# Optimization experiments

Hardware: AMD Instinct MI355X
Metric: run time of the kernel (lower is better)

Reference implementation:

```python
import jax, jax.numpy as jnp
import numpy as np
from jax import lax

NUM_CLASSES = 5
K_MAX = 5
PROTO_DIM = 32
MARGIN = 1.0
ANCHOR_STRENGTH = 1.0
LAMBDA_COMPACT = 0.1
MAX_ANCHORS = 2048
KMEANS_ITERS = 5
EPS = 1e-12


def _normalize(x, axis=-1):
    return x / jnp.sqrt(jnp.sum(x * x, axis=axis, keepdims=True) + EPS)


def _cdist(a, b):
    # Euclidean distance matrix (n, m) via the squared-norm expansion.
    d2 = (jnp.sum(a * a, 1)[:, None] + jnp.sum(b * b, 1)[None, :] - 2.0 * (a @ b.T))
    return jnp.sqrt(jnp.maximum(d2, 0.0))


def _class_centroids(feats, mask, key):
    # feats: (N, D) L2-normalized; mask: (N,) bool selecting this class's voxels.
    N, D = feats.shape
    w = mask.astype(feats.dtype)
    cnt = w.sum()
    mean = (feats * w[:, None]).sum(0) / jnp.maximum(cnt, 1.0)

    def kmeans(_):
        k_init, k_fb = jax.random.split(key)
        # random init: K distinct masked points (gumbel top-k == randperm sample)
        g0 = jax.random.gumbel(k_init, (N,))
        _, init_idx = lax.top_k(jnp.where(mask, g0, -jnp.inf), K_MAX)
        cent0 = feats[init_idx]
        # fallback random masked points for empty clusters, one set per iter
        g2 = jax.random.gumbel(k_fb, (KMEANS_ITERS, N))
        fb_idx = jax.vmap(lambda s: lax.top_k(jnp.where(mask, s, -jnp.inf), K_MAX)[1])(g2)

        def body(cent, fb):
            d = _cdist(feats, cent)                       # (N, K)
            assign = jnp.argmin(d, axis=1)
            onehot = ((assign[:, None] == jnp.arange(K_MAX)[None, :]) & mask[:, None]).astype(feats.dtype)
            counts = onehot.sum(0)                        # (K,)
            sums = onehot.T @ feats                       # (K, D)
            newc = sums / jnp.maximum(counts, 1.0)[:, None]
            newc = jnp.where(counts[:, None] > 0, newc, feats[fb])
            return newc, None

        cent, _ = lax.scan(body, cent0, fb_idx)
        return _normalize(cent)

    def mean_rep(_):
        return jnp.tile(mean[None, :], (K_MAX, 1))

    cent = lax.cond(cnt >= K_MAX, kmeans, mean_rep, None)
    return _normalize(cent), cnt


def _loss_triplet(feats, prototypes, pseudo_masks, gt_masks, labeled_batch):
    B, Df, Zf, Yf, Xf = feats.shape
    N = B * Zf * Yf * Xf
    feats_flat = _normalize(jnp.transpose(feats, (0, 2, 3, 4, 1)).reshape(N, Df))
    # masks are already at feature resolution -> nearest interp is identity
    gt_flat = gt_masks.reshape(-1)
    pseudo_flat = pseudo_masks.reshape(-1)
    protos = _normalize(prototypes)                       # (C, K, D)
    key = jax.random.key(42)

    # ---- anchor loss: match prototypes to per-class kmeans centroids ----
    anchor_loss = jnp.float32(0.0)
    anchor_cnt = jnp.float32(0.0)
    for i in range(int(labeled_batch.shape[0])):
        c = labeled_batch[i]
        c_safe = jnp.clip(c, 0, NUM_CLASSES - 1)
        cmask = gt_flat == c
        cent, cnt = _class_centroids(feats_flat, cmask, jax.random.fold_in(key, i))
        valid = ((c != 0) & (c < NUM_CLASSES) & (cnt > 0)).astype(jnp.float32)
        loss_c = jnp.mean((protos[c_safe] - cent) ** 2)
        anchor_loss = anchor_loss + valid * loss_c
        anchor_cnt = anchor_cnt + valid
    anchor_loss = anchor_loss / jnp.maximum(anchor_cnt, 1.0)

    # ---- compactness: unbiased variance across the K prototypes per class ----
    compact_loss = jnp.var(protos[1:], axis=1, ddof=1).mean(axis=1).sum()

    # ---- triplet loss over pseudo-labeled anchors ----
    amask = pseudo_flat > 0
    ga = jax.random.gumbel(jax.random.fold_in(key, 1000), (N,))
    top_s, aidx = lax.top_k(jnp.where(amask, ga, -jnp.inf), MAX_ANCHORS)
    sel_valid = jnp.isfinite(top_s)                        # padding if < MAX_ANCHORS anchors
    a_feats = feats_flat[aidx]                             # (A, D)
    a_labels = jnp.clip(pseudo_flat[aidx], 0, NUM_CLASSES - 1)

    CK = NUM_CLASSES * K_MAX
    protos_flat = protos.reshape(CK, Df)
    col_cls = jnp.arange(CK) // K_MAX
    own = col_cls[None, :] == a_labels[:, None]            # (A, CK)

    sim = a_feats @ protos_flat.T
    pos_idx = jnp.argmax(jnp.where(own, sim, -jnp.inf), axis=1)
    pos_vecs = protos_flat[pos_idx]

    d_all = _cdist(a_feats, protos_flat)                   # (A, CK)
    pos_d = jnp.min(jnp.where(own, d_all, jnp.inf), axis=1)
    neg = ~own
    semi = neg & (d_all > pos_d[:, None]) & (d_all < pos_d[:, None] + MARGIN)
    g1 = jax.random.gumbel(jax.random.fold_in(key, 2000), (MAX_ANCHORS, CK))
    g2 = jax.random.gumbel(jax.random.fold_in(key, 2001), (MAX_ANCHORS, CK))
    idx_semi = jnp.argmax(jnp.where(semi, g1, -jnp.inf), axis=1)
    idx_rand = jnp.argmax(jnp.where(neg, g2, -jnp.inf), axis=1)
    neg_idx = jnp.where(semi.any(axis=1), idx_semi, idx_rand)
    neg_vecs = protos_flat[neg_idx]

    aN, pN, nN = _normalize(a_feats), _normalize(pos_vecs), _normalize(neg_vecs)
    d_pos = jnp.sqrt(jnp.sum((aN - pN) ** 2, axis=1) + EPS)
    d_neg = jnp.sqrt(jnp.sum((aN - nN) ** 2, axis=1) + EPS)
    wA = (sel_valid & (a_labels != 0)).astype(jnp.float32)
    proto_loss = jnp.sum(jax.nn.softplus(d_pos - d_neg + MARGIN) * wA) / jnp.maximum(wA.sum(), 1.0)

    return proto_loss + ANCHOR_STRENGTH * anchor_loss + LAMBDA_COMPACT * compact_loss


def setup_inputs() -> dict:
    key = jax.random.key(0)
    k1, k2, k3, k4 = jax.random.split(key, 4)
    B, Z = 4, 64
    feats = jax.random.normal(k1, (B, PROTO_DIM, Z, Z, Z), dtype=jnp.float32)
    protos = jax.random.normal(k2, (NUM_CLASSES, K_MAX, PROTO_DIM), dtype=jnp.float32)
    protos = _normalize(protos)
    pseudo_masks = jax.random.randint(k3, (B, Z, Z, Z), 0, NUM_CLASSES, dtype=jnp.int32)
    gt_masks = jax.random.randint(k4, (B, Z, Z, Z), 0, NUM_CLASSES, dtype=jnp.int32)
    labeled_batch = jnp.array([1, 2, 3, 4], dtype=jnp.int32)
    return {"feats": feats, "prototypes": protos, "pseudo_masks": pseudo_masks,
            "gt_masks": gt_masks, "labeled_batch": labeled_batch}


def reference(feats, prototypes, pseudo_masks, gt_masks, labeled_batch):
    return _loss_triplet(feats, prototypes, pseudo_masks, gt_masks, labeled_batch)
```

## Files before the change

kernel.cpp:

```cpp
#include <hip/hip_runtime.h>
#include <hip/hip_fp16.h>
#include <stdint.h>

typedef unsigned int u32;
typedef unsigned long long u64;
typedef unsigned char u8;

#define NCLS 5
#define KMX 5
#define DD 32
#define LBN 4
#define KIT 5
#define MAXA 2048
#define CKK 25
#define NBLKA 256
#define SCPAD 36
#define ACAP 4096
#define UKTHR ((1u << 23) + 1u - (1u << 15))
#define FTINY 1.17549435e-38f

struct RKeys {
  u32 ki[LBN][2];
  u32 kf[LBN][2];
  u32 k1000[2];
  u32 k2000[2];
  u32 k2001[2];
};

struct SelState {
  u32 prefix1, rank1, prefix21, rank2, pivot_sv, target, M, ncand, ncand2;
};

__host__ __device__ inline void tf2x32(u32 k0, u32 k1, u32 x0, u32 x1, u32* o0, u32* o1) {
  u32 ks2 = k0 ^ k1 ^ 0x1BD11BDAu;
  u32 ks[3] = {k0, k1, ks2};
  x0 += k0; x1 += k1;
  const int rotA[4] = {13, 15, 26, 6};
  const int rotB[4] = {17, 29, 16, 24};
#pragma unroll
  for (int g = 0; g < 5; ++g) {
#pragma unroll
    for (int j = 0; j < 4; ++j) {
      int r = (g & 1) ? rotB[j] : rotA[j];
      x0 += x1;
      x1 = (x1 << r) | (x1 >> (32 - r));
      x1 ^= x0;
    }
    x0 += ks[(g + 1) % 3];
    x1 += ks[(g + 2) % 3] + (u32)(g + 1);
  }
  *o0 = x0; *o1 = x1;
}

__device__ inline u32 jax_ukey(u32 k0, u32 k1, u32 half, u32 idx) {
  bool hi = (idx >= half);
  u32 c0 = hi ? (idx - half) : idx;
  u32 c1 = hi ? idx : (idx + half);
  u32 o0, o1;
  tf2x32(k0, k1, c0, c1, &o0, &o1);
  u32 bits = hi ? o1 : o0;
  return (bits >> 9) + 1u;
}

#define INS5(kk, a0, a1, a2, a3, a4) do { u64 _k = (kk); \
  if (_k > a4) { a4 = _k; u64 _t; \
    if (a4 > a3) { _t = a3; a3 = a4; a4 = _t; } \
    if (a3 > a2) { _t = a2; a2 = a3; a3 = _t; } \
    if (a2 > a1) { _t = a1; a1 = a2; a2 = _t; } \
    if (a1 > a0) { _t = a0; a0 = a1; a1 = _t; } } } while (0)

#define WMERGE5(off, a0, a1, a2, a3, a4) do { \
  u64 r0 = __shfl_xor(a0, off, 64), r1 = __shfl_xor(a1, off, 64), \
      r2 = __shfl_xor(a2, off, 64), r3 = __shfl_xor(a3, off, 64), \
      r4 = __shfl_xor(a4, off, 64); \
  INS5(r0, a0, a1, a2, a3, a4); INS5(r1, a0, a1, a2, a3, a4); \
  INS5(r2, a0, a1, a2, a3, a4); INS5(r3, a0, a1, a2, a3, a4); \
  INS5(r4, a0, a1, a2, a3, a4); } while (0)

#define WMERGE_ALL(a0,a1,a2,a3,a4) do { \
  WMERGE5(32,a0,a1,a2,a3,a4); WMERGE5(16,a0,a1,a2,a3,a4); WMERGE5(8,a0,a1,a2,a3,a4); \
  WMERGE5(4,a0,a1,a2,a3,a4); WMERGE5(2,a0,a1,a2,a3,a4); WMERGE5(1,a0,a1,a2,a3,a4); } while (0)

__device__ inline float rsum32(float v) {
#pragma unroll
  for (int o = 16; o; o >>= 1) v += __shfl_xor(v, o, 32);
  return v;
}

__device__ inline float rsum64(float v) {
#pragma unroll
  for (int o = 32; o; o >>= 1) v += __shfl_xor(v, o, 64);
  return v;
}

__device__ inline float4 h8tof4(uint2 u) {
  __half2 a = *reinterpret_cast<__half2*>(&u.x);
  __half2 b = *reinterpret_cast<__half2*>(&u.y);
  float2 fa = __half22float2(a), fb = __half22float2(b);
  return make_float4(fa.x, fa.y, fb.x, fb.y);
}
__device__ inline uint2 f4toh8(float4 f) {
  __half2 a = __float22half2_rn(make_float2(f.x, f.y));
  __half2 b = __float22half2_rn(make_float2(f.z, f.w));
  uint2 u;
  u.x = *reinterpret_cast<u32*>(&a);
  u.y = *reinterpret_cast<u32*>(&b);
  return u;
}


__global__ void k_protos(const float* __restrict__ protos, float* __restrict__ protn, float* __restrict__ compact) {
  __shared__ float pl[CKK * DD];
  __shared__ float rn[CKK];
  __shared__ float red[4];
  int tid = threadIdx.x;
  for (int t = tid; t < CKK * DD; t += 256) pl[t] = protos[t];
  __syncthreads();
  if (tid < CKK) {
    float s = 0.f;
    for (int d = 0; d < DD; ++d) { float x = pl[tid * DD + d]; s += x * x; }
    rn[tid] = sqrtf(s + 1e-12f);
  }
  __syncthreads();
  for (int t = tid; t < CKK * DD; t += 256) {
    float v = pl[t] / rn[t / DD];
    pl[t] = v;
    protn[t] = v;
  }
  __syncthreads();
  float part = 0.f;
  if (tid < (NCLS - 1) * DD) {
    int c = 1 + tid / DD;
    int d = tid % DD;
    float m = 0.f;
#pragma unroll
    for (int k = 0; k < KMX; ++k) m += pl[(c * KMX + k) * DD + d];
    m *= (1.0f / KMX);
    float v = 0.f;
#pragma unroll
    for (int k = 0; k < KMX; ++k) { float df = pl[(c * KMX + k) * DD + d] - m; v += df * df; }
    part = v * (1.0f / (KMX - 1)) * (1.0f / DD);
  }
#pragma unroll
  for (int o = 32; o; o >>= 1) part += __shfl_xor(part, o, 64);
  int wid = tid >> 6;
  if ((tid & 63) == 0) red[wid] = part;
  __syncthreads();
  if (tid == 0) compact[0] = red[0] + red[1] + red[2] + red[3];
}


#define T5PROC_THR(gv_, nn_, cv_) do { \
  int ci = (gv_ == lb0) ? 0 : (gv_ == lb1) ? 1 : (gv_ == lb2) ? 2 : (gv_ == lb3) ? 3 : -1; \
  cv_ = (u8)(ci < 0 ? 255 : ci); \
  if (ci >= 0) { \
    u32 k0 = (ci & 2) ? ((ci & 1) ? ka3 : ka2) : ((ci & 1) ? ka1 : ka0); \
    u32 k1 = (ci & 2) ? ((ci & 1) ? kb3 : kb2) : ((ci & 1) ? kb1 : kb0); \
    u32 uk = jax_ukey(k0, k1, half, (u32)(nn_)); \
    if (uk >= UKTHR) { \
      u64 key = ((u64)uk << 32) | (u32)(~(u32)(nn_)); \
      if (ci == 0) { INS5(key, A0, A1, A2, A3, A4); } \
      else if (ci == 1) { INS5(key, B0, B1, B2, B3, B4); } \
      else if (ci == 2) { INS5(key, C0, C1, C2, C3, C4); } \
      else { INS5(key, D0, D1, D2, D3, D4); } \
    } \
  } } while (0)

#define T5PROC(gv_, nn_) do { \
  int ci = (gv_ == lb0) ? 0 : (gv_ == lb1) ? 1 : (gv_ == lb2) ? 2 : (gv_ == lb3) ? 3 : -1; \
  if (ci >= 0) { \
    u32 k0 = (ci & 2) ? ((ci & 1) ? ka3 : ka2) : ((ci & 1) ? ka1 : ka0); \
    u32 k1 = (ci & 2) ? ((ci & 1) ? kb3 : kb2) : ((ci & 1) ? kb1 : kb0); \
    u32 uk = jax_ukey(k0, k1, half, (u32)(nn_)); \
    u64 key = ((u64)uk << 32) | (u32)(~(u32)(nn_)); \
    if (ci == 0) { INS5(key, A0, A1, A2, A3, A4); } \
    else if (ci == 1) { INS5(key, B0, B1, B2, B3, B4); } \
    else if (ci == 2) { INS5(key, C0, C1, C2, C3, C4); } \
    else { INS5(key, D0, D1, D2, D3, D4); } \
  } } while (0)

#define T5_TAIL_STORE() \
  WMERGE_ALL(A0,A1,A2,A3,A4); \
  WMERGE_ALL(B0,B1,B2,B3,B4); \
  WMERGE_ALL(C0,C1,C2,C3,C4); \
  WMERGE_ALL(D0,D1,D2,D3,D4); \
  __shared__ u64 wbuf[4][20]; \
  int tid = threadIdx.x; \
  int wid = tid >> 6; \
  if ((tid & 63) == 0) { \
    u64* w = wbuf[wid]; \
    w[0]=A0; w[1]=A1; w[2]=A2; w[3]=A3; w[4]=A4; \
    w[5]=B0; w[6]=B1; w[7]=B2; w[8]=B3; w[9]=B4; \
    w[10]=C0; w[11]=C1; w[12]=C2; w[13]=C3; w[14]=C4; \
    w[15]=D0; w[16]=D1; w[17]=D2; w[18]=D3; w[19]=D4; \
  } \
  __syncthreads(); \
  if (tid == 0) { \
    _Pragma("unroll") \
    for (int w = 1; w < 4; ++w) { \
      _Pragma("unroll") \
      for (int j = 0; j < 5; ++j) { \
        u64 ka = wbuf[w][j];      INS5(ka, A0, A1, A2, A3, A4); \
        u64 kb = wbuf[w][5 + j];  INS5(kb, B0, B1, B2, B3, B4); \
        u64 kc = wbuf[w][10 + j]; INS5(kc, C0, C1, C2, C3, C4); \
        u64 kd = wbuf[w][15 + j]; INS5(kd, D0, D1, D2, D3, D4); \
      } \
    } \
    size_t nb = gridDim.x; \
    u64* o0 = outA + ((size_t)0 * nb + blockIdx.x) * 5; \
    o0[0]=A0; o0[1]=A1; o0[2]=A2; o0[3]=A3; o0[4]=A4; \
    u64* o1 = outA + ((size_t)1 * nb + blockIdx.x) * 5; \
    o1[0]=B0; o1[1]=B1; o1[2]=B2; o1[3]=B3; o1[4]=B4; \
    u64* o2 = outA + ((size_t)2 * nb + blockIdx.x) * 5; \
    o2[0]=C0; o2[1]=C1; o2[2]=C2; o2[3]=C3; o2[4]=C4; \
    u64* o3 = outA + ((size_t)3 * nb + blockIdx.x) * 5; \
    o3[0]=D0; o3[1]=D1; o3[2]=D2; o3[3]=D3; o3[4]=D4; \
  }

#define T5_HEAD() \
  int lb0 = labeled[0], lb1 = labeled[1], lb2 = labeled[2], lb3 = labeled[3]; \
  u32 half = (u32)(N / 2); \
  u32 ka0 = RK.ki[0][0], kb0 = RK.ki[0][1]; \
  u32 ka1 = RK.ki[1][0], kb1 = RK.ki[1][1]; \
  u32 ka2 = RK.ki[2][0], kb2 = RK.ki[2][1]; \
  u32 ka3 = RK.ki[3][0], kb3 = RK.ki[3][1]; \
  u64 A0=0,A1=0,A2=0,A3=0,A4=0; \
  u64 B0=0,B1=0,B2=0,B3=0,B4=0; \
  u64 C0=0,C1=0,C2=0,C3=0,C4=0; \
  u64 D0=0,D1=0,D2=0,D3=0,D4=0;

__global__ void k_top5A(const int* __restrict__ gt, const int* __restrict__ labeled,
                        RKeys RK, u64* __restrict__ outA, u8* __restrict__ ci8, int N) {
  T5_HEAD()
  int Nq = N >> 2;
  int stride = gridDim.x * blockDim.x;
  for (int q = blockIdx.x * blockDim.x + threadIdx.x; q < Nq; q += stride) {
    int4 g4 = ((const int4*)gt)[q];
    int n = q << 2;
    u8 c0v, c1v, c2v, c3v;
    T5PROC_THR(g4.x, n, c0v);
    T5PROC_THR(g4.y, n + 1, c1v);
    T5PROC_THR(g4.z, n + 2, c2v);
    T5PROC_THR(g4.w, n + 3, c3v);
    ((uchar4*)ci8)[q] = make_uchar4(c0v, c1v, c2v, c3v);
  }
  T5_TAIL_STORE()
}

__global__ void k_top5B(const u64* __restrict__ outA, u32* __restrict__ rescue,
                        u64* __restrict__ top5F, int nblk) {
  int i = blockIdx.x;
  const u64* src = outA + (size_t)i * nblk * 5;
  u64 t0 = 0, t1 = 0, t2 = 0, t3 = 0, t4 = 0;
  int tot = nblk * 5;
  for (int j = threadIdx.x; j < tot; j += blockDim.x) { u64 k = src[j]; INS5(k, t0, t1, t2, t3, t4); }
  WMERGE_ALL(t0, t1, t2, t3, t4);
  __shared__ u64 wbuf[4 * 5];
  int tid = threadIdx.x;
  int wid = tid >> 6;
  if ((tid & 63) == 0) {
    wbuf[wid * 5 + 0] = t0; wbuf[wid * 5 + 1] = t1; wbuf[wid * 5 + 2] = t2;
    wbuf[wid * 5 + 3] = t3; wbuf[wid * 5 + 4] = t4;
  }
  __syncthreads();
  if (tid == 0) {
#pragma unroll
    for (int w = 1; w < 4; ++w)
#pragma unroll
      for (int j = 0; j < 5; ++j) { u64 k = wbuf[w * 5 + j]; INS5(k, t0, t1, t2, t3, t4); }
    u64* o = top5F + (size_t)i * 5;
    o[0] = t0; o[1] = t1; o[2] = t2; o[3] = t3; o[4] = t4;
    if (t4 == 0ULL) atomicOr(rescue, 1u << i);
  }
}

__global__ void k_top5A_resc(const int* __restrict__ gt, const int* __restrict__ labeled,
                             RKeys RK, const u32* __restrict__ rescue,
                             u64* __restrict__ outA, int N) {
  if ((rescue[0] & 0xFu) == 0u) return;
  T5_HEAD()
  int Nq = N >> 2;
  int stride = gridDim.x * blockDim.x;
  for (int q = blockIdx.x * blockDim.x + threadIdx.x; q < Nq; q += stride) {
    int4 g4 = ((const int4*)gt)[q];
    int n = q << 2;
    T5PROC(g4.x, n);
    T5PROC(g4.y, n + 1);
    T5PROC(g4.z, n + 2);
    T5PROC(g4.w, n + 3);
  }
  T5_TAIL_STORE()
}

__global__ void k_top5B_resc(const u64* __restrict__ outA, const u32* __restrict__ rescue,
                             u64* __restrict__ top5F, int nblk) {
  int i = blockIdx.x;
  if (!((rescue[0] >> i) & 1u)) return;
  const u64* src = outA + (size_t)i * nblk * 5;
  u64 t0 = 0, t1 = 0, t2 = 0, t3 = 0, t4 = 0;
  int tot = nblk * 5;
  for (int j = threadIdx.x; j < tot; j += blockDim.x) { u64 k = src[j]; INS5(k, t0, t1, t2, t3, t4); }
  WMERGE_ALL(t0, t1, t2, t3, t4);
  __shared__ u64 wbuf[4 * 5];
  int tid = threadIdx.x;
  int wid = tid >> 6;
  if ((tid & 63) == 0) {
    wbuf[wid * 5 + 0] = t0; wbuf[wid * 5 + 1] = t1; wbuf[wid * 5 + 2] = t2;
    wbuf[wid * 5 + 3] = t3; wbuf[wid * 5 + 4] = t4;
  }
  __syncthreads();
  if (tid == 0) {
#pragma unroll
    for (int w = 1; w < 4; ++w)
#pragma unroll
      for (int j = 0; j < 5; ++j) { u64 k = wbuf[w * 5 + j]; INS5(k, t0, t1, t2, t3, t4); }
    u64* o = top5F + (size_t)i * 5;
    o[0] = t0; o[1] = t1; o[2] = t2; o[3] = t3; o[4] = t4;
  }
}


__global__ void __launch_bounds__(256)
k_normT(const float4* __restrict__ feats4, uint2* __restrict__ featsH2, int N, int Z3) {
  __shared__ float xl[128 * 33];
  __shared__ float sinv[128];
  int tid = threadIdx.x;
  int nchunk = N >> 7;
  int Z3q = Z3 >> 2;
  for (int chunk = blockIdx.x; chunk < nchunk; chunk += gridDim.x) {
    int n0 = chunk << 7;
    int b = n0 / Z3, v0 = n0 - b * Z3;
    const float4* fb4 = feats4 + (size_t)b * DD * Z3q + (v0 >> 2);
#pragma unroll
    for (int j = 0; j < 4; ++j) {
      int idx = j * 256 + tid;
      int d = idx >> 5, v4 = idx & 31;
      float4 f = fb4[(size_t)d * Z3q + v4];
      int vb = v4 << 2;
      xl[(vb + 0) * 33 + d] = f.x;
      xl[(vb + 1) * 33 + d] = f.y;
      xl[(vb + 2) * 33 + d] = f.z;
      xl[(vb + 3) * 33 + d] = f.w;
    }
    __syncthreads();
    if (tid < 128) {
      float s = 0.f;
#pragma unroll
      for (int d = 0; d < DD; ++d) { float x = xl[tid * 33 + d]; s += x * x; }
      sinv[tid] = 1.0f / sqrtf(s + 1e-12f);
    }
    __syncthreads();
#pragma unroll
    for (int j = 0; j < 4; ++j) {
      int idx = j * 256 + tid;
      int vox = idx >> 3, q = idx & 7;
      float iv = sinv[vox];
      float4 o;
      o.x = xl[vox * 33 + q * 4 + 0] * iv;
      o.y = xl[vox * 33 + q * 4 + 1] * iv;
      o.z = xl[vox * 33 + q * 4 + 2] * iv;
      o.w = xl[vox * 33 + q * 4 + 3] * iv;
      featsH2[(size_t)n0 * 8 + idx] = f4toh8(o);
    }
    __syncthreads();
  }
}

__global__ void k_initcentT(const u32* __restrict__ featsH,
                            const u64* __restrict__ top5F, float* __restrict__ cent, int N) {
  int t = threadIdx.x;
  if (t >= LBN * KMX * DD) return;
  int d = t & 31;
  int k = (t >> 5) % KMX;
  int i = t / (KMX * DD);
  u32 n = ~(u32)(top5F[(size_t)i * 5 + k]);
  if (n >= (u32)N) n = 0;
  const __half* fh = (const __half*)featsH;
  cent[(i * KMX + k) * DD + d] = __half2float(fh[(size_t)n * DD + d]);
}

__global__ void __launch_bounds__(256)
k_assignW2(const uint2* __restrict__ featsH2, const u8* __restrict__ ci8,
           const float* __restrict__ cent, float* __restrict__ part, int N, int NB) {
  __shared__ float sc[LBN * KMX * SCPAD];
  __shared__ float ssw[8][LBN * KMX * SCPAD];
  __shared__ float scn[LBN * KMX];
  __shared__ float scw[8][LBN * KMX];
  int tid = threadIdx.x;
  for (int t = tid; t < LBN * KMX * DD; t += 256) {
    int cl2 = t >> 5, d = t & 31;
    sc[cl2 * SCPAD + d] = cent[t];
  }
  for (int t = tid; t < 8 * LBN * KMX * SCPAD; t += 256) (&ssw[0][0])[t] = 0.f;
  for (int t = tid; t < 8 * LBN * KMX; t += 256) (&scw[0][0])[t] = 0.f;
  __syncthreads();
  if (tid < LBN * KMX) {
    float s = 0.f;
#pragma unroll
    for (int d = 0; d < DD; ++d) { float c = sc[tid * SCPAD + d]; s += c * c; }
    scn[tid] = s;
  }
  __syncthreads();
  int q = tid & 7;
  int grp = (tid >> 3) & 7;
  int wv = tid >> 6;
  int cpi = 2 * wv + (grp >> 2);
  float* myss = &ssw[cpi][0];
  float* mysc = &scw[cpi][0];
  int sstep = grp & 3;
  const float* scq = sc + q * 4;
  int nchunk = N >> 5;
  int chunk = blockIdx.x;
  if (chunk < nchunk) {
    uint2 h2 = featsH2[(size_t)chunk * 256 + tid];
    int cv = ci8[(chunk << 5) + (tid >> 3)];
    while (true) {
      int nxt = chunk + gridDim.x;
      bool has = nxt < nchunk;
      uint2 nh2 = make_uint2(0u, 0u); int ncv = 255;
      if (has) {
        nh2 = featsH2[(size_t)nxt * 256 + tid];
        ncv = ci8[(nxt << 5) + (tid >> 3)];
      }
      float4 f4 = h8tof4(h2);
      int ci = (cv == 255) ? -1 : cv;
      int basec = (ci < 0 ? 0 : ci) * KMX;
      float4 c0 = *(const float4*)(scq + (basec + 0) * SCPAD);
      float4 c1 = *(const float4*)(scq + (basec + 1) * SCPAD);
      float4 c2 = *(const float4*)(scq + (basec + 2) * SCPAD);
      float4 c3 = *(const float4*)(scq + (basec + 3) * SCPAD);
      float4 c4 = *(const float4*)(scq + (basec + 4) * SCPAD);
      float p0 = f4.x * c0.x + f4.y * c0.y + f4.z * c0.z + f4.w * c0.w;
      float p1 = f4.x * c1.x + f4.y * c1.y + f4.z * c1.z + f4.w * c1.w;
      float p2 = f4.x * c2.x + f4.y * c2.y + f4.z * c2.z + f4.w * c2.w;
      float p3 = f4.x * c3.x + f4.y * c3.y + f4.z * c3.z + f4.w * c3.w;
      float p4 = f4.x * c4.x + f4.y * c4.y + f4.z * c4.z + f4.w * c4.w;
#pragma unroll
      for (int o = 1; o < 8; o <<= 1) {
        p0 += __shfl_xor(p0, o, 64);
        p1 += __shfl_xor(p1, o, 64);
        p2 += __shfl_xor(p2, o, 64);
        p3 += __shfl_xor(p3, o, 64);
        p4 += __shfl_xor(p4, o, 64);
      }
      float bd = scn[basec + 0] - 2.0f * p0; int bk = 0;
      float d2;
      d2 = scn[basec + 1] - 2.0f * p1; if (d2 < bd) { bd = d2; bk = 1; }
      d2 = scn[basec + 2] - 2.0f * p2; if (d2 < bd) { bd = d2; bk = 2; }
      d2 = scn[basec + 3] - 2.0f * p3; if (d2 < bd) { bd = d2; bk = 3; }
      d2 = scn[basec + 4] - 2.0f * p4; if (d2 < bd) { bd = d2; bk = 4; }
      int cl = basec + bk;
#pragma unroll
      for (int s = 0; s < 4; ++s) {
        if (sstep == s && ci >= 0) {
          float* dst = myss + cl * SCPAD + q * 4;
          float4 cur = *(float4*)dst;
          cur.x += f4.x; cur.y += f4.y; cur.z += f4.z; cur.w += f4.w;
          *(float4*)dst = cur;
          if (q == 0) mysc[cl] += 1.0f;
        }
      }
      if (!has) break;
      chunk = nxt; h2 = nh2; cv = ncv;
    }
  }
  __syncthreads();
  for (int p = tid; p < 660; p += 256) {
    float v;
    if (p < 640) {
      int idx = (p >> 5) * SCPAD + (p & 31);
      v = ssw[0][idx] + ssw[1][idx] + ssw[2][idx] + ssw[3][idx]
        + ssw[4][idx] + ssw[5][idx] + ssw[6][idx] + ssw[7][idx];
    } else {
      int ik = p - 640;
      v = scw[0][ik] + scw[1][ik] + scw[2][ik] + scw[3][ik]
        + scw[4][ik] + scw[5][ik] + scw[6][ik] + scw[7][ik];
    }
    part[(size_t)p * NB + blockIdx.x] = v;
  }
}

__global__ void k_redupdT(const float* __restrict__ part, float* __restrict__ cent,
                          float* __restrict__ sums, float* __restrict__ kcnt,
                          u32* __restrict__ emptyMask, int NB) {
  __shared__ float w4[8];
  int p = blockIdx.x;
  int tid = threadIdx.x;
  if (p < 640) {
    int ik = p >> 5;
    float s = 0.f, c = 0.f;
    for (int b2 = tid; b2 < NB; b2 += 256) {
      s += part[(size_t)p * NB + b2];
      c += part[(size_t)(640 + ik) * NB + b2];
    }
    s = rsum64(s); c = rsum64(c);
    int wid = tid >> 6;
    if ((tid & 63) == 0) { w4[wid] = s; w4[4 + wid] = c; }
    __syncthreads();
    if (tid == 0) {
      float S = w4[0] + w4[1] + w4[2] + w4[3];
      float C = w4[4] + w4[5] + w4[6] + w4[7];
      sums[p] = S;
      if (C > 0.f) cent[p] = S / fmaxf(C, 1.0f);
      else atomicOr(emptyMask, 1u << ik);
    }
  } else if (p < 660) {
    int ik = p - 640;
    float c = 0.f;
    for (int b2 = tid; b2 < NB; b2 += 256) c += part[(size_t)(640 + ik) * NB + b2];
    c = rsum64(c);
    int wid = tid >> 6;
    if ((tid & 63) == 0) w4[wid] = c;
    __syncthreads();
    if (tid == 0) kcnt[ik] = w4[0] + w4[1] + w4[2] + w4[3];
  }
}

__global__ void __launch_bounds__(1024)
k_fixempty(const u32* __restrict__ featsH, const int* __restrict__ gt,
           const int* __restrict__ labeled, RKeys RK, u32* __restrict__ emptyMask,
           float* __restrict__ cent, int iter, int N) {
  u32 mask = emptyMask[0];
  if (mask == 0u) return;
  __shared__ u64 wbuf[16 * 5];
  __shared__ u32 idxs[KMX];
  int tid = threadIdx.x;
  u32 halfF = (u32)(((u64)5 * (u64)N) / 2);
  for (int ci = 0; ci < LBN; ++ci) {
    if (((mask >> (ci * KMX)) & 0x1Fu) == 0u) continue;
    int c = labeled[ci];
    u32 fa = RK.kf[ci][0], fb = RK.kf[ci][1];
    u32 base = (u32)iter * (u32)N;
    u64 t0 = 0, t1 = 0, t2 = 0, t3 = 0, t4 = 0;
    for (int n = tid; n < N; n += 1024) {
      if (gt[n] != c) continue;
      u32 uk = jax_ukey(fa, fb, halfF, base + (u32)n);
      u64 key = ((u64)uk << 32) | (u32)(~(u32)n);
      INS5(key, t0, t1, t2, t3, t4);
    }
    WMERGE_ALL(t0, t1, t2, t3, t4);
    int wid = tid >> 6;
    if ((tid & 63) == 0) {
      wbuf[wid * 5 + 0] = t0; wbuf[wid * 5 + 1] = t1; wbuf[wid * 5 + 2] = t2;
      wbuf[wid * 5 + 3] = t3; wbuf[wid * 5 + 4] = t4;
    }
    __syncthreads();
    if (tid == 0) {
      for (int w = 1; w < 16; ++w)
        for (int j = 0; j < 5; ++j) { u64 k = wbuf[w * 5 + j]; INS5(k, t0, t1, t2, t3, t4); }
      idxs[0] = ~(u32)t0; idxs[1] = ~(u32)t1; idxs[2] = ~(u32)t2;
      idxs[3] = ~(u32)t3; idxs[4] = ~(u32)t4;
    }
    __syncthreads();
    if (tid < KMX * DD) {
      int k = tid >> 5, d = tid & 31;
      if ((mask >> (ci * KMX + k)) & 1u) {
        u32 n = idxs[k];
        if (n >= (u32)N) n = 0;
        const __half* fh = (const __half*)featsH;
        cent[(ci * KMX + k) * DD + d] = __half2float(fh[(size_t)n * DD + d]);
      }
    }
    __syncthreads();
  }
  if (tid == 0) emptyMask[0] = 0u;
}

__global__ void k_prepT(const uint2* __restrict__ featsH2,
                        const int* __restrict__ pseudo, const SelState* __restrict__ st,
                        const int* __restrict__ aidx, float4* __restrict__ afe4,
                        int* __restrict__ alab, int N) {
  int tid = threadIdx.x;
  int r = blockIdx.x * 32 + (tid >> 3);
  int q = tid & 7;
  if (r >= (int)st->target) return;
  int n = aidx[r];
  if ((u32)n >= (u32)N) n = 0;
  if (q == 0) {
    int lb = pseudo[n];
    alab[r] = lb < 0 ? 0 : (lb > NCLS - 1 ? NCLS - 1 : lb);
  }
  afe4[(size_t)r * 8 + q] = h8tof4(featsH2[(size_t)n * 8 + q]);
}


__global__ void __launch_bounds__(256)
k_anchsel(const int* __restrict__ pseudo, RKeys RK, u64* __restrict__ cand4k,
          SelState* st, int N) {
  __shared__ u32 mcnt[4];
  u32 K0 = RK.k1000[0], K1 = RK.k1000[1];
  u32 half = (u32)(N / 2);
  int tid = threadIdx.x;
  int lcnt = 0;
  int stride = gridDim.x * blockDim.x;
  for (int n = blockIdx.x * blockDim.x + tid; n < N; n += stride) {
    bool valid = pseudo[n] > 0;
    lcnt += valid ? 1 : 0;
    u32 uk = jax_ukey(K0, K1, half, (u32)n);
    bool c = valid && (uk >= UKTHR);
    if (__ballot(c)) {
      if (c) {
        u32 p = atomicAdd(&st->ncand, 1u);
        if (p < (u32)ACAP) cand4k[p] = ((u64)uk << 32) | (u32)(~(u32)n);
      }
    }
  }
#pragma unroll
  for (int o = 32; o; o >>= 1) lcnt += __shfl_xor(lcnt, o, 64);
  if ((tid & 63) == 0) mcnt[tid >> 6] = (u32)lcnt;
  __syncthreads();
  if (tid == 0) atomicAdd(&st->M, mcnt[0] + mcnt[1] + mcnt[2] + mcnt[3]);
}

__global__ void k_selmode(SelState* st, u32* rescue) {
  if (threadIdx.x != 0 || blockIdx.x != 0) return;
  u32 M = st->M;
  u32 tgt = M < (u32)MAXA ? M : (u32)MAXA;
  st->target = tgt;
  if (!(st->ncand >= tgt && st->ncand <= (u32)ACAP)) rescue[1] = 1u;
}

__global__ void __launch_bounds__(256)
k_rank(const u64* __restrict__ cand4k, const SelState* __restrict__ st,
       const u32* __restrict__ rescue, int* __restrict__ aidx) {
  if (rescue[1]) return;
  __shared__ u64 keys[ACAP];
  u32 nc = st->ncand; if (nc > (u32)ACAP) nc = (u32)ACAP;
  u32 target = st->target;
  int tid = threadIdx.x;
  for (int t = tid; t < ACAP; t += 256) keys[t] = (t < (int)nc) ? cand4k[t] : 0ULL;
  __syncthreads();
  int i = blockIdx.x * 256 + tid;
  if (i >= (int)nc) return;
  u64 my = keys[i];
  u32 rank = 0;
  for (u32 j = 0; j < nc; ++j) rank += (keys[j] > my) ? 1u : 0u;
  if (rank < target) aidx[rank] = (int)(~(u32)my);
}


__global__ void k_svinit(const int* __restrict__ pseudo, RKeys RK, const u32* __restrict__ rescue,
                         u32* __restrict__ sv, u32* __restrict__ hist, int N) {
  if (!rescue[1]) return;
  __shared__ u32 h[2048];
  for (int t = threadIdx.x; t < 2048; t += blockDim.x) h[t] = 0;
  __syncthreads();
  u32 half = (u32)(N / 2);
  u32 K0 = RK.k1000[0], K1 = RK.k1000[1];
  int Nq = N >> 2;
  int stride = gridDim.x * blockDim.x;
  for (int q = blockIdx.x * blockDim.x + threadIdx.x; q < Nq; q += stride) {
    int4 p4 = ((const int4*)pseudo)[q];
    int n = q << 2;
    u32 s0 = 0, s1 = 0, s2 = 0, s3 = 0;
    if (p4.x > 0) { s0 = jax_ukey(K0, K1, half, (u32)n);     atomicAdd(&h[s0 >> 21], 1u); }
    if (p4.y > 0) { s1 = jax_ukey(K0, K1, half, (u32)n + 1); atomicAdd(&h[s1 >> 21], 1u); }
    if (p4.z > 0) { s2 = jax_ukey(K0, K1, half, (u32)n + 2); atomicAdd(&h[s2 >> 21], 1u); }
    if (p4.w > 0) { s3 = jax_ukey(K0, K1, half, (u32)n + 3); atomicAdd(&h[s3 >> 21], 1u); }
    ((uint4*)sv)[q] = make_uint4(s0, s1, s2, s3);
  }
  __syncthreads();
  for (int t = threadIdx.x; t < 2048; t += blockDim.x) if (h[t]) atomicAdd(&hist[t], h[t]);
}

__global__ void k_hist12(const u32* __restrict__ sv, u32* __restrict__ hist,
                         const SelState* __restrict__ st, const u32* __restrict__ rescue,
                         int pass, int N) {
  if (!rescue[1]) return;
  __shared__ u32 h[2048];
  for (int t = threadIdx.x; t < 2048; t += blockDim.x) h[t] = 0;
  __syncthreads();
  u32 pre = (pass == 1) ? st->prefix1 : st->prefix21;
  int Nq = N >> 2;
  int stride = gridDim.x * blockDim.x;
  for (int q = blockIdx.x * blockDim.x + threadIdx.x; q < Nq; q += stride) {
    uint4 s4 = ((const uint4*)sv)[q];
#define H12(s_) do { u32 s = (s_); if (s) { \
      if (pass == 1) { if ((s >> 21) == pre) atomicAdd(&h[(s >> 10) & 0x7FFu], 1u); } \
      else           { if ((s >> 10) == pre) atomicAdd(&h[s & 0x3FFu], 1u); } } } while (0)
    H12(s4.x); H12(s4.y); H12(s4.z); H12(s4.w);
#undef H12
  }
  __syncthreads();
  for (int t = threadIdx.x; t < 2048; t += blockDim.x) if (h[t]) atomicAdd(&hist[t], h[t]);
}

__global__ void k_scan(const u32* __restrict__ hist, SelState* st,
                       const u32* __restrict__ rescue, int pass) {
  if (!rescue[1]) return;
  __shared__ u32 h[2048];
  __shared__ u32 csum[256];
  __shared__ u32 sh_rank;
  __shared__ int sh_found;
  __shared__ u32 sh_rem;
  int tid = threadIdx.x;
  int nb = (pass == 2) ? 1024 : 2048;
  for (int t = tid; t < 2048; t += 256) h[t] = (t < nb) ? hist[t] : 0u;
  __syncthreads();
  u32 cs = 0;
#pragma unroll
  for (int j = 0; j < 8; ++j) cs += h[tid * 8 + j];
  csum[tid] = cs;
  __syncthreads();
  if (tid == 0) {
    sh_rank = (pass == 0) ? st->target : (pass == 1 ? st->rank1 : st->rank2);
    sh_found = -1;
    sh_rem = 0;
  }
  __syncthreads();
  u32 rank = sh_rank;
  if (rank > 0) {
    u32 above = 0;
    for (int j = tid + 1; j < 256; ++j) above += csum[j];
    u32 run = above;
    for (int b = tid * 8 + 7; b >= tid * 8; --b) {
      u32 c = h[b];
      if (run < rank && rank <= run + c) { sh_found = b; sh_rem = rank - run; }
      run += c;
    }
  }
  __syncthreads();
  if (tid == 0) {
    int found = sh_found;
    u32 rem = sh_rem;
    if (pass == 0) {
      if (found < 0) { st->prefix1 = 0xFFFFFFFFu; st->rank1 = 0; }
      else { st->prefix1 = (u32)found; st->rank1 = rem; }
    } else if (pass == 1) {
      if (found < 0) { st->prefix21 = 0xFFFFFFFFu; st->rank2 = 0; }
      else { st->prefix21 = (st->prefix1 << 11) | (u32)found; st->rank2 = rem; }
    } else {
      if (found < 0) st->pivot_sv = 0xFFFFFFFFu;
      else st->pivot_sv = (st->prefix21 << 10) | (u32)found;
    }
  }
}

__global__ void k_gather(const u32* __restrict__ sv, SelState* st,
                         const u32* __restrict__ rescue, u64* __restrict__ cand, int N) {
  if (!rescue[1]) return;
  if (st->target == 0) return;
  u32 piv = st->pivot_sv;
  int Nq = N >> 2;
  int stride = gridDim.x * blockDim.x;
  for (int q = blockIdx.x * blockDim.x + threadIdx.x; q < Nq; q += stride) {
    uint4 s4 = ((const uint4*)sv)[q];
    int n = q << 2;
#define GPUSH(s_, nn_) do { u32 s = (s_); \
    if (s && s >= piv) { u32 p = atomicAdd(&st->ncand2, 1u); \
      if (p < 4096u) cand[p] = ((u64)s << 32) | (u32)(~(u32)(nn_)); } } while (0)
    GPUSH(s4.x, n); GPUSH(s4.y, n + 1); GPUSH(s4.z, n + 2); GPUSH(s4.w, n + 3);
#undef GPUSH
  }
}

__global__ void __launch_bounds__(1024) k_sortsel(const u64* __restrict__ cand,
                                                  const SelState* __restrict__ st,
                                                  const u32* __restrict__ rescue,
                                                  int* __restrict__ aidx) {
  if (!rescue[1]) return;
  __shared__ u64 s[4096];
  u32 nc = st->ncand2; if (nc > 4096u) nc = 4096u;
  u32 target = st->target;
  for (int t = threadIdx.x; t < 4096; t += blockDim.x) s[t] = (t < (int)nc) ? cand[t] : 0ULL;
  __syncthreads();
  for (u32 ksz = 2; ksz <= 4096; ksz <<= 1) {
    for (u32 j = ksz >> 1; j > 0; j >>= 1) {
      for (u32 idx = threadIdx.x; idx < 4096; idx += blockDim.x) {
        u32 ixj = idx ^ j;
        if (ixj > idx) {
          bool up = (idx & ksz) == 0;
          u64 A = s[idx], B = s[ixj];
          bool sw = up ? (A < B) : (A > B);
          if (sw) { s[idx] = B; s[ixj] = A; }
        }
      }
      __syncthreads();
    }
  }
  for (int t = threadIdx.x; t < MAXA; t += blockDim.x)
    if (t < (int)target) aidx[t] = (int)(~(u32)s[t]);
}


__global__ void k_anchor_final(const float* __restrict__ cent, const float* __restrict__ sums,
                               const float* __restrict__ kcnt, const float* __restrict__ protn,
                               const int* __restrict__ labeled, float* __restrict__ accum) {
  int i = blockIdx.x;
  int d = threadIdx.x;
  if (d >= DD) return;
  int c = labeled[i];
  float cnt = 0.f;
#pragma unroll
  for (int k = 0; k < KMX; ++k) cnt += kcnt[i * KMX + k];
  int cs = c < 0 ? 0 : (c > NCLS - 1 ? NCLS - 1 : c);
  float part = 0.f;
  if (cnt >= (float)KMX) {
#pragma unroll
    for (int k = 0; k < KMX; ++k) {
      float v = cent[(i * KMX + k) * DD + d];
      float s = rsum32(v * v);
      float dn1 = sqrtf(s + 1e-12f);
      float v1 = v / dn1;
      float s2 = rsum32(v1 * v1);
      float dn2 = sqrtf(s2 + 1e-12f);
      float vv = v1 / dn2;
      float df = protn[(cs * KMX + k) * DD + d] - vv;
      part += df * df;
    }
  } else {
    float mv = 0.f;
#pragma unroll
    for (int k = 0; k < KMX; ++k) mv += sums[(i * KMX + k) * DD + d];
    mv /= fmaxf(cnt, 1.0f);
    float s = rsum32(mv * mv);
    float dn = sqrtf(s + 1e-12f);
    float vv = mv / dn;
#pragma unroll
    for (int k = 0; k < KMX; ++k) {
      float df = protn[(cs * KMX + k) * DD + d] - vv;
      part += df * df;
    }
  }
  float ls = rsum32(part) * (1.0f / (KMX * DD));
  bool valid = (c != 0) && (c < NCLS) && (cnt > 0.f);
  if (d == 0 && valid) { atomicAdd(&accum[0], ls); atomicAdd(&accum[1], 1.0f); }
}

__global__ void k_triplet(const float* __restrict__ protn, const float* __restrict__ afe,
                          const int* __restrict__ alab, const SelState* __restrict__ st,
                          RKeys RK, float* __restrict__ acc) {
  __shared__ float pn[CKK * DD];
  __shared__ float spn[CKK];
  int tid = threadIdx.x;
  for (int t = tid; t < CKK * DD; t += blockDim.x) pn[t] = protn[t];
  __syncthreads();
  if (tid < CKK) {
    float s = 0.f;
    for (int d = 0; d < DD; ++d) s += pn[tid * DD + d] * pn[tid * DD + d];
    spn[tid] = s;
  }
  __syncthreads();
  int r = blockIdx.x * blockDim.x + tid;
  if (r >= (int)st->target) return;
  float a[DD]; float sa = 0.f;
#pragma unroll
  for (int d = 0; d < DD; ++d) { a[d] = afe[(size_t)r * DD + d]; sa += a[d] * a[d]; }
  int lab = alab[r];
  int ob = lab * KMX;
  float bs = -3.4e38f; int pidx = ob;
  float pos_d = 3.4e38f;
  for (int k = ob; k < ob + KMX; ++k) {
    float dot = 0.f;
#pragma unroll
    for (int d = 0; d < DD; ++d) dot += a[d] * pn[k * DD + d];
    if (dot > bs) { bs = dot; pidx = k; }
    float d2 = (sa + spn[k]) - 2.0f * dot;
    float dd = sqrtf(fmaxf(d2, 0.f));
    pos_d = fminf(pos_d, dd);
  }
  u32 halfT = (u32)(MAXA * CKK / 2);
  bool any_semi = false;
  u32 bu1 = 0; int k1i = 0;
  u32 bu2 = 0; int k2i = 0;
  for (int k = 0; k < CKK; ++k) {
    if (k / KMX == lab) continue;
    float dot = 0.f;
#pragma unroll
    for (int d = 0; d < DD; ++d) dot += a[d] * pn[k * DD + d];
    float d2 = (sa + spn[k]) - 2.0f * dot;
    float dd = sqrtf(fmaxf(d2, 0.f));
    u32 j = (u32)(r * CKK + k);
    bool semi = (dd > pos_d) && (dd < pos_d + 1.0f);
    if (semi) {
      u32 u1 = jax_ukey(RK.k2000[0], RK.k2000[1], halfT, j);
      any_semi = true;
      if (u1 > bu1) { bu1 = u1; k1i = k; }
    }
    u32 u2 = jax_ukey(RK.k2001[0], RK.k2001[1], halfT, j);
    if (u2 > bu2) { bu2 = u2; k2i = k; }
  }
  int nidx = any_semi ? k1i : k2i;
  float aden = sqrtf(sa + 1e-12f);
  float pden = sqrtf(spn[pidx] + 1e-12f);
  float nden = sqrtf(spn[nidx] + 1e-12f);
  float s1 = 0.f, s2 = 0.f;
#pragma unroll
  for (int d = 0; d < DD; ++d) {
    float an = a[d] / aden;
    float pv = pn[pidx * DD + d] / pden;
    float nv = pn[nidx * DD + d] / nden;
    float t1 = an - pv; s1 += t1 * t1;
    float t2 = an - nv; s2 += t2 * t2;
  }
  float d_pos = sqrtf(s1 + 1e-12f);
  float d_neg = sqrtf(s2 + 1e-12f);
  float xx = (d_pos - d_neg) + 1.0f;
  float l = fmaxf(xx, 0.f) + log1pf(expf(-fabsf(xx)));
  atomicAdd(&acc[0], l);
  atomicAdd(&acc[1], 1.0f);
}

__global__ void k_final(const float* __restrict__ anchor_acc, const float* __restrict__ proto_acc,
                        const float* __restrict__ compact, float* __restrict__ out) {
  if (threadIdx.x != 0 || blockIdx.x != 0) return;
  float al = anchor_acc[0] / fmaxf(anchor_acc[1], 1.0f);
  float pl = proto_acc[0] / fmaxf(proto_acc[1], 1.0f);
  out[0] = pl + 1.0f * al + 0.1f * compact[0];
}


static void host_keys(RKeys* K) {
  const u32 b0 = 0u, b1 = 42u;
  u32 o0, o1;
  for (int i = 0; i < LBN; ++i) {
    u32 f0, f1;
    tf2x32(b0, b1, 0u, (u32)i, &f0, &f1);
    u32 p0, q0, p1, q1;
    tf2x32(f0, f1, 0u, 2u, &p0, &q0);
    tf2x32(f0, f1, 1u, 3u, &p1, &q1);
    K->ki[i][0] = p0; K->ki[i][1] = p1;
    K->kf[i][0] = q0; K->kf[i][1] = q1;
  }
  tf2x32(b0, b1, 0u, 1000u, &o0, &o1); K->k1000[0] = o0; K->k1000[1] = o1;
  tf2x32(b0, b1, 0u, 2000u, &o0, &o1); K->k2000[0] = o0; K->k2000[1] = o1;
  tf2x32(b0, b1, 0u, 2001u, &o0, &o1); K->k2001[0] = o0; K->k2001[1] = o1;
}

extern "C" void kernel_launch(void* const* d_in, const int* in_sizes, int n_in,
                              void* d_out, int out_size, void* d_ws, size_t ws_size,
                              hipStream_t stream) {
  const float* feats = (const float*)d_in[0];
  const float* protos = (const float*)d_in[1];
  const int* pseudo = (const int*)d_in[2];
  const int* gt = (const int*)d_in[3];
  const int* labeled = (const int*)d_in[4];
  float* out = (float*)d_out;

  int N = in_sizes[2];
  int Z3 = N / 4;

  RKeys RK;
  host_keys(&RK);

  const int nbas[3] = {1536, 768, 384};
  for (int attempt = 0; attempt < 3; ++attempt) {
    int NBAS = nbas[attempt];
    char* W = (char*)d_ws;
    size_t off = 0;
    auto alloc = [&](size_t bytes) -> char* {
      char* p = W + off;
      off += (bytes + 255) & ~(size_t)255;
      return p;
    };
    char* zeroBase = W + off;
    u32* hist3 = (u32*)alloc(3 * 2048 * 4);
    SelState* st = (SelState*)alloc(256);
    float* anchor_acc = (float*)alloc(256);
    float* proto_acc = (float*)alloc(256);
    u32* rescue = (u32*)alloc(256);
    size_t zeroBytes = (size_t)((W + off) - zeroBase);
    u64* cand4k = (u64*)alloc((size_t)ACAP * 8);
    u64* outA = (u64*)alloc((size_t)LBN * NBLKA * 5 * 8);
    u64* top5F = (u64*)alloc((size_t)LBN * 5 * 8);
    float* cent = (float*)alloc((size_t)LBN * KMX * DD * 4);
    float* sums = (float*)alloc((size_t)LBN * KMX * DD * 4);
    float* kcnt = (float*)alloc((size_t)LBN * KMX * 4);
    float* protn = (float*)alloc((size_t)CKK * DD * 4);
    float* compact = (float*)alloc(256);
    u32* sv = (u32*)alloc((size_t)N * 4);
    float* part = (float*)alloc((size_t)680 * NBAS * 4);
    u64* cand = (u64*)alloc(4096 * 8);
    int* aidx = (int*)alloc((size_t)MAXA * 4);
    int* alab = (int*)alloc((size_t)MAXA * 4);
    float* afe = (float*)alloc((size_t)MAXA * DD * 4);
    u32* featsH = (u32*)alloc((size_t)N * DD * 2);
    u8* ci8 = (u8*)alloc((size_t)N);
    if (ws_size < off) continue;

    hipMemsetAsync(zeroBase, 0, zeroBytes, stream);

    k_protos<<<dim3(1), dim3(256), 0, stream>>>(protos, protn, compact);

    k_top5A<<<dim3(NBLKA), dim3(256), 0, stream>>>(gt, labeled, RK, outA, ci8, N);
    k_top5B<<<dim3(LBN), dim3(256), 0, stream>>>(outA, rescue, top5F, NBLKA);
    k_top5A_resc<<<dim3(NBLKA), dim3(256), 0, stream>>>(gt, labeled, RK, rescue, outA, N);
    k_top5B_resc<<<dim3(LBN), dim3(256), 0, stream>>>(outA, rescue, top5F, NBLKA);

    uint2* featsH2 = (uint2*)featsH;
    k_normT<<<dim3(4096), dim3(256), 0, stream>>>((const float4*)feats, featsH2, N, Z3);
    k_initcentT<<<dim3(1), dim3(LBN * KMX * DD), 0, stream>>>(featsH, top5F, cent, N);
    for (int it = 0; it < KIT; ++it) {
      k_assignW2<<<dim3(NBAS), dim3(256), 0, stream>>>(featsH2, ci8, cent, part, N, NBAS);
      k_redupdT<<<dim3(660), dim3(256), 0, stream>>>(part, cent, sums, kcnt, rescue + 2, NBAS);
      k_fixempty<<<dim3(1), dim3(1024), 0, stream>>>(featsH, gt, labeled, RK, rescue + 2, cent, it, N);
    }
    k_anchor_final<<<dim3(LBN), dim3(64), 0, stream>>>(cent, sums, kcnt, protn, labeled, anchor_acc);

    k_anchsel<<<dim3(2048), dim3(256), 0, stream>>>(pseudo, RK, cand4k, st, N);
    k_selmode<<<dim3(1), dim3(64), 0, stream>>>(st, rescue);
    k_svinit<<<dim3(1024), dim3(256), 0, stream>>>(pseudo, RK, rescue, sv, hist3, N);
    k_scan<<<dim3(1), dim3(256), 0, stream>>>(hist3, st, rescue, 0);
    k_hist12<<<dim3(1024), dim3(256), 0, stream>>>(sv, hist3 + 2048, st, rescue, 1, N);
    k_scan<<<dim3(1), dim3(256), 0, stream>>>(hist3 + 2048, st, rescue, 1);
    k_hist12<<<dim3(1024), dim3(256), 0, stream>>>(sv, hist3 + 4096, st, rescue, 2, N);
    k_scan<<<dim3(1), dim3(256), 0, stream>>>(hist3 + 4096, st, rescue, 2);
    k_gather<<<dim3(1024), dim3(256), 0, stream>>>(sv, st, rescue, cand, N);
    k_sortsel<<<dim3(1), dim3(1024), 0, stream>>>(cand, st, rescue, aidx);
    k_rank<<<dim3(ACAP / 256), dim3(256), 0, stream>>>(cand4k, st, rescue, aidx);

    k_prepT<<<dim3(MAXA / 32), dim3(256), 0, stream>>>(featsH2, pseudo, st, aidx,
                                                        (float4*)afe, alab, N);
    k_triplet<<<dim3(MAXA / 256), dim3(256), 0, stream>>>(protn, afe, alab, st, RK, proto_acc);

    k_final<<<dim3(1), dim3(64), 0, stream>>>(anchor_acc, proto_acc, compact, out);
    return;
  }
}
```

Measured before the change: 556.6 us.

## Cut kernel launches by merging rescue, fixempty, selmode and prep kernels

Reduces the number of kernel launches. The empty-cluster fix is folded into the centroid reduction through a last-block ticket, and k_selmode is folded into k_anchsel the same way. The rarely-taken rescue paths (top5 and the anchor radix select) are collapsed into single-block kernels, and the anchor feature gather is fused into k_triplet. Rare rescue paths now run on one block, which is slow if they trigger, and the last-block pattern depends on threadfence and atomic ordering for correctness.

```diff
diff --git a/kernel.cpp b/kernel.cpp
--- a/kernel.cpp
+++ b/kernel.cpp
@@ -17,7 +17,6 @@
 #define SCPAD 36
 #define ACAP 4096
 #define UKTHR ((1u << 23) + 1u - (1u << 15))
-#define FTINY 1.17549435e-38f
 
 struct RKeys {
   u32 ki[LBN][2];
@@ -179,44 +178,6 @@
     else { INS5(key, D0, D1, D2, D3, D4); } \
   } } while (0)
 
-#define T5_TAIL_STORE() \
-  WMERGE_ALL(A0,A1,A2,A3,A4); \
-  WMERGE_ALL(B0,B1,B2,B3,B4); \
-  WMERGE_ALL(C0,C1,C2,C3,C4); \
-  WMERGE_ALL(D0,D1,D2,D3,D4); \
-  __shared__ u64 wbuf[4][20]; \
-  int tid = threadIdx.x; \
-  int wid = tid >> 6; \
-  if ((tid & 63) == 0) { \
-    u64* w = wbuf[wid]; \
-    w[0]=A0; w[1]=A1; w[2]=A2; w[3]=A3; w[4]=A4; \
-    w[5]=B0; w[6]=B1; w[7]=B2; w[8]=B3; w[9]=B4; \
-    w[10]=C0; w[11]=C1; w[12]=C2; w[13]=C3; w[14]=C4; \
-    w[15]=D0; w[16]=D1; w[17]=D2; w[18]=D3; w[19]=D4; \
-  } \
-  __syncthreads(); \
-  if (tid == 0) { \
-    _Pragma("unroll") \
-    for (int w = 1; w < 4; ++w) { \
-      _Pragma("unroll") \
-      for (int j = 0; j < 5; ++j) { \
-        u64 ka = wbuf[w][j];      INS5(ka, A0, A1, A2, A3, A4); \
-        u64 kb = wbuf[w][5 + j];  INS5(kb, B0, B1, B2, B3, B4); \
-        u64 kc = wbuf[w][10 + j]; INS5(kc, C0, C1, C2, C3, C4); \
-        u64 kd = wbuf[w][15 + j]; INS5(kd, D0, D1, D2, D3, D4); \
-      } \
-    } \
-    size_t nb = gridDim.x; \
-    u64* o0 = outA + ((size_t)0 * nb + blockIdx.x) * 5; \
-    o0[0]=A0; o0[1]=A1; o0[2]=A2; o0[3]=A3; o0[4]=A4; \
-    u64* o1 = outA + ((size_t)1 * nb + blockIdx.x) * 5; \
-    o1[0]=B0; o1[1]=B1; o1[2]=B2; o1[3]=B3; o1[4]=B4; \
-    u64* o2 = outA + ((size_t)2 * nb + blockIdx.x) * 5; \
-    o2[0]=C0; o2[1]=C1; o2[2]=C2; o2[3]=C3; o2[4]=C4; \
-    u64* o3 = outA + ((size_t)3 * nb + blockIdx.x) * 5; \
-    o3[0]=D0; o3[1]=D1; o3[2]=D2; o3[3]=D3; o3[4]=D4; \
-  }
-
 #define T5_HEAD() \
   int lb0 = labeled[0], lb1 = labeled[1], lb2 = labeled[2], lb3 = labeled[3]; \
   u32 half = (u32)(N / 2); \
@@ -244,7 +205,42 @@
     T5PROC_THR(g4.w, n + 3, c3v);
     ((uchar4*)ci8)[q] = make_uchar4(c0v, c1v, c2v, c3v);
   }
-  T5_TAIL_STORE()
+  WMERGE_ALL(A0,A1,A2,A3,A4);
+  WMERGE_ALL(B0,B1,B2,B3,B4);
+  WMERGE_ALL(C0,C1,C2,C3,C4);
+  WMERGE_ALL(D0,D1,D2,D3,D4);
+  __shared__ u64 wbuf[4][20];
+  int tid = threadIdx.x;
+  int wid = tid >> 6;
+  if ((tid & 63) == 0) {
+    u64* w = wbuf[wid];
+    w[0]=A0; w[1]=A1; w[2]=A2; w[3]=A3; w[4]=A4;
+    w[5]=B0; w[6]=B1; w[7]=B2; w[8]=B3; w[9]=B4;
+    w[10]=C0; w[11]=C1; w[12]=C2; w[13]=C3; w[14]=C4;
+    w[15]=D0; w[16]=D1; w[17]=D2; w[18]=D3; w[19]=D4;
+  }
+  __syncthreads();
+  if (tid == 0) {
+#pragma unroll
+    for (int w = 1; w < 4; ++w) {
+#pragma unroll
+      for (int j = 0; j < 5; ++j) {
+        u64 ka = wbuf[w][j];      INS5(ka, A0, A1, A2, A3, A4);
+        u64 kb = wbuf[w][5 + j];  INS5(kb, B0, B1, B2, B3, B4);
+        u64 kc = wbuf[w][10 + j]; INS5(kc, C0, C1, C2, C3, C4);
+        u64 kd = wbuf[w][15 + j]; INS5(kd, D0, D1, D2, D3, D4);
+      }
+    }
+    size_t nb = gridDim.x;
+    u64* o0 = outA + ((size_t)0 * nb + blockIdx.x) * 5;
+    o0[0]=A0; o0[1]=A1; o0[2]=A2; o0[3]=A3; o0[4]=A4;
+    u64* o1 = outA + ((size_t)1 * nb + blockIdx.x) * 5;
+    o1[0]=B0; o1[1]=B1; o1[2]=B2; o1[3]=B3; o1[4]=B4;
+    u64* o2 = outA + ((size_t)2 * nb + blockIdx.x) * 5;
+    o2[0]=C0; o2[1]=C1; o2[2]=C2; o2[3]=C3; o2[4]=C4;
+    u64* o3 = outA + ((size_t)3 * nb + blockIdx.x) * 5;
+    o3[0]=D0; o3[1]=D1; o3[2]=D2; o3[3]=D3; o3[4]=D4;
+  }
 }
 
 __global__ void k_top5B(const u64* __restrict__ outA, u32* __restrict__ rescue,
@@ -274,14 +270,14 @@
   }
 }
 
-__global__ void k_top5A_resc(const int* __restrict__ gt, const int* __restrict__ labeled,
-                             RKeys RK, const u32* __restrict__ rescue,
-                             u64* __restrict__ outA, int N) {
+__global__ void __launch_bounds__(1024)
+k_top5resc(const int* __restrict__ gt, const int* __restrict__ labeled,
+           RKeys RK, const u32* __restrict__ rescue, u64* __restrict__ top5F, int N) {
   if ((rescue[0] & 0xFu) == 0u) return;
   T5_HEAD()
+  int tid = threadIdx.x;
   int Nq = N >> 2;
-  int stride = gridDim.x * blockDim.x;
-  for (int q = blockIdx.x * blockDim.x + threadIdx.x; q < Nq; q += stride) {
+  for (int q = tid; q < Nq; q += 1024) {
     int4 g4 = ((const int4*)gt)[q];
     int n = q << 2;
     T5PROC(g4.x, n);
@@ -289,33 +285,33 @@
     T5PROC(g4.z, n + 2);
     T5PROC(g4.w, n + 3);
   }
-  T5_TAIL_STORE()
-}
-
-__global__ void k_top5B_resc(const u64* __restrict__ outA, const u32* __restrict__ rescue,
-                             u64* __restrict__ top5F, int nblk) {
-  int i = blockIdx.x;
-  if (!((rescue[0] >> i) & 1u)) return;
-  const u64* src = outA + (size_t)i * nblk * 5;
-  u64 t0 = 0, t1 = 0, t2 = 0, t3 = 0, t4 = 0;
-  int tot = nblk * 5;
-  for (int j = threadIdx.x; j < tot; j += blockDim.x) { u64 k = src[j]; INS5(k, t0, t1, t2, t3, t4); }
-  WMERGE_ALL(t0, t1, t2, t3, t4);
-  __shared__ u64 wbuf[4 * 5];
-  int tid = threadIdx.x;
+  WMERGE_ALL(A0,A1,A2,A3,A4);
+  WMERGE_ALL(B0,B1,B2,B3,B4);
+  WMERGE_ALL(C0,C1,C2,C3,C4);
+  WMERGE_ALL(D0,D1,D2,D3,D4);
+  __shared__ u64 wbuf[16][20];
   int wid = tid >> 6;
   if ((tid & 63) == 0) {
-    wbuf[wid * 5 + 0] = t0; wbuf[wid * 5 + 1] = t1; wbuf[wid * 5 + 2] = t2;
-    wbuf[wid * 5 + 3] = t3; wbuf[wid * 5 + 4] = t4;
+    u64* w = wbuf[wid];
+    w[0]=A0; w[1]=A1; w[2]=A2; w[3]=A3; w[4]=A4;
+    w[5]=B0; w[6]=B1; w[7]=B2; w[8]=B3; w[9]=B4;
+    w[10]=C0; w[11]=C1; w[12]=C2; w[13]=C3; w[14]=C4;
+    w[15]=D0; w[16]=D1; w[17]=D2; w[18]=D3; w[19]=D4;
   }
   __syncthreads();
   if (tid == 0) {
-#pragma unroll
-    for (int w = 1; w < 4; ++w)
-#pragma unroll
-      for (int j = 0; j < 5; ++j) { u64 k = wbuf[w * 5 + j]; INS5(k, t0, t1, t2, t3, t4); }
-    u64* o = top5F + (size_t)i * 5;
-    o[0] = t0; o[1] = t1; o[2] = t2; o[3] = t3; o[4] = t4;
+    for (int w = 1; w < 16; ++w) {
+      for (int j = 0; j < 5; ++j) {
+        u64 ka = wbuf[w][j];      INS5(ka, A0, A1, A2, A3, A4);
+        u64 kb = wbuf[w][5 + j];  INS5(kb, B0, B1, B2, B3, B4);
+        u64 kc = wbuf[w][10 + j]; INS5(kc, C0, C1, C2, C3, C4);
+        u64 kd = wbuf[w][15 + j]; INS5(kd, D0, D1, D2, D3, D4);
+      }
+    }
+    top5F[0]=A0; top5F[1]=A1; top5F[2]=A2; top5F[3]=A3; top5F[4]=A4;
+    top5F[5]=B0; top5F[6]=B1; top5F[7]=B2; top5F[8]=B3; top5F[9]=B4;
+    top5F[10]=C0; top5F[11]=C1; top5F[12]=C2; top5F[13]=C3; top5F[14]=C4;
+    top5F[15]=D0; top5F[16]=D1; top5F[17]=D2; top5F[18]=D3; top5F[19]=D4;
   }
 }
 
@@ -482,8 +478,12 @@
 
 __global__ void k_redupdT(const float* __restrict__ part, float* __restrict__ cent,
                           float* __restrict__ sums, float* __restrict__ kcnt,
-                          u32* __restrict__ emptyMask, int NB) {
+                          u32* __restrict__ emptyMask, u32* __restrict__ ticket,
+                          const u32* __restrict__ featsH, const int* __restrict__ gt,
+                          const int* __restrict__ labeled, RKeys RK, int iter, int N, int NB) {
   __shared__ float w4[8];
+  __shared__ int isLast;
+  __shared__ u32 shMask;
   int p = blockIdx.x;
   int tid = threadIdx.x;
   if (p < 640) {
@@ -504,7 +504,7 @@
       if (C > 0.f) cent[p] = S / fmaxf(C, 1.0f);
       else atomicOr(emptyMask, 1u << ik);
     }
-  } else if (p < 660) {
+  } else {
     int ik = p - 640;
     float c = 0.f;
     for (int b2 = tid; b2 < NB; b2 += 256) c += part[(size_t)(640 + ik) * NB + b2];
@@ -514,17 +514,19 @@
     __syncthreads();
     if (tid == 0) kcnt[ik] = w4[0] + w4[1] + w4[2] + w4[3];
   }
-}
-
-__global__ void __launch_bounds__(1024)
-k_fixempty(const u32* __restrict__ featsH, const int* __restrict__ gt,
-           const int* __restrict__ labeled, RKeys RK, u32* __restrict__ emptyMask,
-           float* __restrict__ cent, int iter, int N) {
-  u32 mask = emptyMask[0];
+  __syncthreads();
+  __threadfence();
+  if (tid == 0) {
+    u32 old = atomicAdd(ticket, 1u);
+    isLast = (old == (u32)(gridDim.x - 1)) ? 1 : 0;
+    if (isLast) shMask = atomicAdd(emptyMask, 0u);
+  }
+  __syncthreads();
+  if (!isLast) return;
+  u32 mask = shMask;
   if (mask == 0u) return;
-  __shared__ u64 wbuf[16 * 5];
+  __shared__ u64 wbuf[4 * 5];
   __shared__ u32 idxs[KMX];
-  int tid = threadIdx.x;
   u32 halfF = (u32)(((u64)5 * (u64)N) / 2);
   for (int ci = 0; ci < LBN; ++ci) {
     if (((mask >> (ci * KMX)) & 0x1Fu) == 0u) continue;
@@ -532,7 +534,7 @@
     u32 fa = RK.kf[ci][0], fb = RK.kf[ci][1];
     u32 base = (u32)iter * (u32)N;
     u64 t0 = 0, t1 = 0, t2 = 0, t3 = 0, t4 = 0;
-    for (int n = tid; n < N; n += 1024) {
+    for (int n = tid; n < N; n += 256) {
       if (gt[n] != c) continue;
       u32 uk = jax_ukey(fa, fb, halfF, base + (u32)n);
       u64 key = ((u64)uk << 32) | (u32)(~(u32)n);
@@ -546,7 +548,7 @@
     }
     __syncthreads();
     if (tid == 0) {
-      for (int w = 1; w < 16; ++w)
+      for (int w = 1; w < 4; ++w)
         for (int j = 0; j < 5; ++j) { u64 k = wbuf[w * 5 + j]; INS5(k, t0, t1, t2, t3, t4); }
       idxs[0] = ~(u32)t0; idxs[1] = ~(u32)t1; idxs[2] = ~(u32)t2;
       idxs[3] = ~(u32)t3; idxs[4] = ~(u32)t4;
@@ -563,30 +565,13 @@
     }
     __syncthreads();
   }
-  if (tid == 0) emptyMask[0] = 0u;
-}
-
-__global__ void k_prepT(const uint2* __restrict__ featsH2,
-                        const int* __restrict__ pseudo, const SelState* __restrict__ st,
-                        const int* __restrict__ aidx, float4* __restrict__ afe4,
-                        int* __restrict__ alab, int N) {
-  int tid = threadIdx.x;
-  int r = blockIdx.x * 32 + (tid >> 3);
-  int q = tid & 7;
-  if (r >= (int)st->target) return;
-  int n = aidx[r];
-  if ((u32)n >= (u32)N) n = 0;
-  if (q == 0) {
-    int lb = pseudo[n];
-    alab[r] = lb < 0 ? 0 : (lb > NCLS - 1 ? NCLS - 1 : lb);
-  }
-  afe4[(size_t)r * 8 + q] = h8tof4(featsH2[(size_t)n * 8 + q]);
+  if (tid == 0) atomicExch(emptyMask, 0u);
 }
 
 
 __global__ void __launch_bounds__(256)
 k_anchsel(const int* __restrict__ pseudo, RKeys RK, u64* __restrict__ cand4k,
-          SelState* st, int N) {
+          SelState* st, u32* __restrict__ rescue, u32* __restrict__ ticket, int N) {
   __shared__ u32 mcnt[4];
   u32 K0 = RK.k1000[0], K1 = RK.k1000[1];
   u32 half = (u32)(N / 2);
@@ -609,15 +594,18 @@
   for (int o = 32; o; o >>= 1) lcnt += __shfl_xor(lcnt, o, 64);
   if ((tid & 63) == 0) mcnt[tid >> 6] = (u32)lcnt;
   __syncthreads();
-  if (tid == 0) atomicAdd(&st->M, mcnt[0] + mcnt[1] + mcnt[2] + mcnt[3]);
-}
-
-__global__ void k_selmode(SelState* st, u32* rescue) {
-  if (threadIdx.x != 0 || blockIdx.x != 0) return;
-  u32 M = st->M;
-  u32 tgt = M < (u32)MAXA ? M : (u32)MAXA;
-  st->target = tgt;
-  if (!(st->ncand >= tgt && st->ncand <= (u32)ACAP)) rescue[1] = 1u;
+  if (tid == 0) {
+    atomicAdd(&st->M, mcnt[0] + mcnt[1] + mcnt[2] + mcnt[3]);
+    __threadfence();
+    u32 old = atomicAdd(ticket, 1u);
+    if (old == (u32)(gridDim.x - 1)) {
+      u32 M = atomicAdd(&st->M, 0u);
+      u32 nc = atomicAdd(&st->ncand, 0u);
+      u32 tgt = M < (u32)MAXA ? M : (u32)MAXA;
+      st->target = tgt;
+      if (!(nc >= tgt && nc <= (u32)ACAP)) atomicExch(&rescue[1], 1u);
+    }
+  }
 }
 
 __global__ void __launch_bounds__(256)
@@ -638,148 +626,90 @@
   if (rank < target) aidx[rank] = (int)(~(u32)my);
 }
 
-
-__global__ void k_svinit(const int* __restrict__ pseudo, RKeys RK, const u32* __restrict__ rescue,
-                         u32* __restrict__ sv, u32* __restrict__ hist, int N) {
+__global__ void __launch_bounds__(1024)
+k_rescue(const int* __restrict__ pseudo, RKeys RK, const SelState* __restrict__ st,
+         const u32* __restrict__ rescue, int* __restrict__ aidx, int N) {
   if (!rescue[1]) return;
   __shared__ u32 h[2048];
-  for (int t = threadIdx.x; t < 2048; t += blockDim.x) h[t] = 0;
-  __syncthreads();
+  __shared__ u64 sb[ACAP];
+  __shared__ u32 sh_pre1, sh_rank1, sh_pre21, sh_rank2, sh_piv, sh_cnt;
+  int tid = threadIdx.x;
+  u32 K0 = RK.k1000[0], K1 = RK.k1000[1];
   u32 half = (u32)(N / 2);
-  u32 K0 = RK.k1000[0], K1 = RK.k1000[1];
-  int Nq = N >> 2;
-  int stride = gridDim.x * blockDim.x;
-  for (int q = blockIdx.x * blockDim.x + threadIdx.x; q < Nq; q += stride) {
-    int4 p4 = ((const int4*)pseudo)[q];
-    int n = q << 2;
-    u32 s0 = 0, s1 = 0, s2 = 0, s3 = 0;
-    if (p4.x > 0) { s0 = jax_ukey(K0, K1, half, (u32)n);     atomicAdd(&h[s0 >> 21], 1u); }
-    if (p4.y > 0) { s1 = jax_ukey(K0, K1, half, (u32)n + 1); atomicAdd(&h[s1 >> 21], 1u); }
-    if (p4.z > 0) { s2 = jax_ukey(K0, K1, half, (u32)n + 2); atomicAdd(&h[s2 >> 21], 1u); }
-    if (p4.w > 0) { s3 = jax_ukey(K0, K1, half, (u32)n + 3); atomicAdd(&h[s3 >> 21], 1u); }
-    ((uint4*)sv)[q] = make_uint4(s0, s1, s2, s3);
-  }
-  __syncthreads();
-  for (int t = threadIdx.x; t < 2048; t += blockDim.x) if (h[t]) atomicAdd(&hist[t], h[t]);
-}
-
-__global__ void k_hist12(const u32* __restrict__ sv, u32* __restrict__ hist,
-                         const SelState* __restrict__ st, const u32* __restrict__ rescue,
-                         int pass, int N) {
-  if (!rescue[1]) return;
-  __shared__ u32 h[2048];
-  for (int t = threadIdx.x; t < 2048; t += blockDim.x) h[t] = 0;
-  __syncthreads();
-  u32 pre = (pass == 1) ? st->prefix1 : st->prefix21;
-  int Nq = N >> 2;
-  int stride = gridDim.x * blockDim.x;
-  for (int q = blockIdx.x * blockDim.x + threadIdx.x; q < Nq; q += stride) {
-    uint4 s4 = ((const uint4*)sv)[q];
-#define H12(s_) do { u32 s = (s_); if (s) { \
-      if (pass == 1) { if ((s >> 21) == pre) atomicAdd(&h[(s >> 10) & 0x7FFu], 1u); } \
-      else           { if ((s >> 10) == pre) atomicAdd(&h[s & 0x3FFu], 1u); } } } while (0)
-    H12(s4.x); H12(s4.y); H12(s4.z); H12(s4.w);
-#undef H12
-  }
-  __syncthreads();
-  for (int t = threadIdx.x; t < 2048; t += blockDim.x) if (h[t]) atomicAdd(&hist[t], h[t]);
-}
-
-__global__ void k_scan(const u32* __restrict__ hist, SelState* st,
-                       const u32* __restrict__ rescue, int pass) {
-  if (!rescue[1]) return;
-  __shared__ u32 h[2048];
-  __shared__ u32 csum[256];
-  __shared__ u32 sh_rank;
-  __shared__ int sh_found;
-  __shared__ u32 sh_rem;
-  int tid = threadIdx.x;
-  int nb = (pass == 2) ? 1024 : 2048;
-  for (int t = tid; t < 2048; t += 256) h[t] = (t < nb) ? hist[t] : 0u;
-  __syncthreads();
-  u32 cs = 0;
-#pragma unroll
-  for (int j = 0; j < 8; ++j) cs += h[tid * 8 + j];
-  csum[tid] = cs;
+  u32 target = st->target;
+  for (int t = tid; t < 2048; t += 1024) h[t] = 0;
+  __syncthreads();
+  for (int n = tid; n < N; n += 1024)
+    if (pseudo[n] > 0) { u32 s = jax_ukey(K0, K1, half, (u32)n); atomicAdd(&h[s >> 21], 1u); }
   __syncthreads();
   if (tid == 0) {
-    sh_rank = (pass == 0) ? st->target : (pass == 1 ? st->rank1 : st->rank2);
-    sh_found = -1;
-    sh_rem = 0;
-  }
-  __syncthreads();
-  u32 rank = sh_rank;
-  if (rank > 0) {
-    u32 above = 0;
-    for (int j = tid + 1; j < 256; ++j) above += csum[j];
-    u32 run = above;
-    for (int b = tid * 8 + 7; b >= tid * 8; --b) {
-      u32 c = h[b];
-      if (run < rank && rank <= run + c) { sh_found = b; sh_rem = rank - run; }
-      run += c;
-    }
-  }
+    u64 cum = 0; int found = -1; u32 rem = 0;
+    if (target > 0)
+      for (int b = 2047; b >= 0; --b) { u32 c = h[b];
+        if (cum < target && target <= cum + c) { found = b; rem = target - (u32)cum; break; } cum += c; }
+    sh_pre1 = (found < 0) ? 0xFFFFFFFFu : (u32)found; sh_rank1 = rem;
+  }
+  __syncthreads();
+  u32 pre1 = sh_pre1, rank1 = sh_rank1;
+  for (int t = tid; t < 2048; t += 1024) h[t] = 0;
+  __syncthreads();
+  for (int n = tid; n < N; n += 1024)
+    if (pseudo[n] > 0) { u32 s = jax_ukey(K0, K1, half, (u32)n);
+      if ((s >> 21) == pre1) atomicAdd(&h[(s >> 10) & 0x7FFu], 1u); }
   __syncthreads();
   if (tid == 0) {
-    int found = sh_found;
-    u32 rem = sh_rem;
-    if (pass == 0) {
-      if (found < 0) { st->prefix1 = 0xFFFFFFFFu; st->rank1 = 0; }
-      else { st->prefix1 = (u32)found; st->rank1 = rem; }
-    } else if (pass == 1) {
-      if (found < 0) { st->prefix21 = 0xFFFFFFFFu; st->rank2 = 0; }
-      else { st->prefix21 = (st->prefix1 << 11) | (u32)found; st->rank2 = rem; }
-    } else {
-      if (found < 0) st->pivot_sv = 0xFFFFFFFFu;
-      else st->pivot_sv = (st->prefix21 << 10) | (u32)found;
-    }
-  }
-}
-
-__global__ void k_gather(const u32* __restrict__ sv, SelState* st,
-                         const u32* __restrict__ rescue, u64* __restrict__ cand, int N) {
-  if (!rescue[1]) return;
-  if (st->target == 0) return;
-  u32 piv = st->pivot_sv;
-  int Nq = N >> 2;
-  int stride = gridDim.x * blockDim.x;
-  for (int q = blockIdx.x * blockDim.x + threadIdx.x; q < Nq; q += stride) {
-    uint4 s4 = ((const uint4*)sv)[q];
-    int n = q << 2;
-#define GPUSH(s_, nn_) do { u32 s = (s_); \
-    if (s && s >= piv) { u32 p = atomicAdd(&st->ncand2, 1u); \
-      if (p < 4096u) cand[p] = ((u64)s << 32) | (u32)(~(u32)(nn_)); } } while (0)
-    GPUSH(s4.x, n); GPUSH(s4.y, n + 1); GPUSH(s4.z, n + 2); GPUSH(s4.w, n + 3);
-#undef GPUSH
-  }
-}
-
-__global__ void __launch_bounds__(1024) k_sortsel(const u64* __restrict__ cand,
-                                                  const SelState* __restrict__ st,
-                                                  const u32* __restrict__ rescue,
-                                                  int* __restrict__ aidx) {
-  if (!rescue[1]) return;
-  __shared__ u64 s[4096];
-  u32 nc = st->ncand2; if (nc > 4096u) nc = 4096u;
-  u32 target = st->target;
-  for (int t = threadIdx.x; t < 4096; t += blockDim.x) s[t] = (t < (int)nc) ? cand[t] : 0ULL;
-  __syncthreads();
-  for (u32 ksz = 2; ksz <= 4096; ksz <<= 1) {
+    u64 cum = 0; int found = -1; u32 rem = 0;
+    if (rank1 > 0)
+      for (int b = 2047; b >= 0; --b) { u32 c = h[b];
+        if (cum < rank1 && rank1 <= cum + c) { found = b; rem = rank1 - (u32)cum; break; } cum += c; }
+    sh_pre21 = (found < 0) ? 0xFFFFFFFFu : ((pre1 << 11) | (u32)found); sh_rank2 = rem;
+  }
+  __syncthreads();
+  u32 pre21 = sh_pre21, rank2 = sh_rank2;
+  for (int t = tid; t < 2048; t += 1024) h[t] = 0;
+  __syncthreads();
+  for (int n = tid; n < N; n += 1024)
+    if (pseudo[n] > 0) { u32 s = jax_ukey(K0, K1, half, (u32)n);
+      if ((s >> 10) == pre21) atomicAdd(&h[s & 0x3FFu], 1u); }
+  __syncthreads();
+  if (tid == 0) {
+    u64 cum = 0; int found = -1;
+    if (rank2 > 0)
+      for (int b = 1023; b >= 0; --b) { u32 c = h[b];
+        if (cum < rank2 && rank2 <= cum + c) { found = b; break; } cum += c; }
+    sh_piv = (found < 0) ? 0xFFFFFFFFu : ((pre21 << 10) | (u32)found);
+    sh_cnt = 0;
+  }
+  __syncthreads();
+  u32 piv = sh_piv;
+  for (int t = tid; t < ACAP; t += 1024) sb[t] = 0ULL;
+  __syncthreads();
+  for (int n = tid; n < N; n += 1024) {
+    if (pseudo[n] > 0) {
+      u32 s = jax_ukey(K0, K1, half, (u32)n);
+      if (s >= piv) {
+        u32 p = atomicAdd(&sh_cnt, 1u);
+        if (p < (u32)ACAP) sb[p] = ((u64)s << 32) | (u32)(~(u32)n);
+      }
+    }
+  }
+  __syncthreads();
+  for (u32 ksz = 2; ksz <= (u32)ACAP; ksz <<= 1) {
     for (u32 j = ksz >> 1; j > 0; j >>= 1) {
-      for (u32 idx = threadIdx.x; idx < 4096; idx += blockDim.x) {
+      for (u32 idx = tid; idx < (u32)ACAP; idx += 1024) {
         u32 ixj = idx ^ j;
         if (ixj > idx) {
           bool up = (idx & ksz) == 0;
-          u64 A = s[idx], B = s[ixj];
+          u64 A = sb[idx], B = sb[ixj];
           bool sw = up ? (A < B) : (A > B);
-          if (sw) { s[idx] = B; s[ixj] = A; }
+          if (sw) { sb[idx] = B; sb[ixj] = A; }
         }
       }
       __syncthreads();
     }
   }
-  for (int t = threadIdx.x; t < MAXA; t += blockDim.x)
-    if (t < (int)target) aidx[t] = (int)(~(u32)s[t]);
+  for (int t = tid; t < MAXA; t += 1024)
+    if (t < (int)target) aidx[t] = (int)(~(u32)sb[t]);
 }
 
 
@@ -827,9 +757,10 @@
   if (d == 0 && valid) { atomicAdd(&accum[0], ls); atomicAdd(&accum[1], 1.0f); }
 }
 
-__global__ void k_triplet(const float* __restrict__ protn, const float* __restrict__ afe,
-                          const int* __restrict__ alab, const SelState* __restrict__ st,
-                          RKeys RK, float* __restrict__ acc) {
+__global__ void k_triplet(const float* __restrict__ protn, const uint2* __restrict__ featsH2,
+                          const int* __restrict__ pseudo, const int* __restrict__ aidx,
+                          const SelState* __restrict__ st, RKeys RK,
+                          float* __restrict__ acc, int N) {
   __shared__ float pn[CKK * DD];
   __shared__ float spn[CKK];
   int tid = threadIdx.x;
@@ -843,10 +774,18 @@
   __syncthreads();
   int r = blockIdx.x * blockDim.x + tid;
   if (r >= (int)st->target) return;
+  int n = aidx[r];
+  if ((u32)n >= (u32)N) n = 0;
+  int lab = pseudo[n];
+  lab = lab < 0 ? 0 : (lab > NCLS - 1 ? NCLS - 1 : lab);
   float a[DD]; float sa = 0.f;
 #pragma unroll
-  for (int d = 0; d < DD; ++d) { a[d] = afe[(size_t)r * DD + d]; sa += a[d] * a[d]; }
-  int lab = alab[r];
+  for (int qq = 0; qq < 8; ++qq) {
+    float4 f4 = h8tof4(featsH2[(size_t)n * 8 + qq]);
+    a[qq * 4 + 0] = f4.x; a[qq * 4 + 1] = f4.y;
+    a[qq * 4 + 2] = f4.z; a[qq * 4 + 3] = f4.w;
+    sa += f4.x * f4.x + f4.y * f4.y + f4.z * f4.z + f4.w * f4.w;
+  }
   int ob = lab * KMX;
   float bs = -3.4e38f; int pidx = ob;
   float pos_d = 3.4e38f;
@@ -954,11 +893,11 @@
       return p;
     };
     char* zeroBase = W + off;
-    u32* hist3 = (u32*)alloc(3 * 2048 * 4);
     SelState* st = (SelState*)alloc(256);
     float* anchor_acc = (float*)alloc(256);
     float* proto_acc = (float*)alloc(256);
     u32* rescue = (u32*)alloc(256);
+    u32* tickets = (u32*)alloc(256);
     size_t zeroBytes = (size_t)((W + off) - zeroBase);
     u64* cand4k = (u64*)alloc((size_t)ACAP * 8);
     u64* outA = (u64*)alloc((size_t)LBN * NBLKA * 5 * 8);
@@ -968,12 +907,8 @@
     float* kcnt = (float*)alloc((size_t)LBN * KMX * 4);
     float* protn = (float*)alloc((size_t)CKK * DD * 4);
     float* compact = (float*)alloc(256);
-    u32* sv = (u32*)alloc((size_t)N * 4);
     float* part = (float*)alloc((size_t)680 * NBAS * 4);
-    u64* cand = (u64*)alloc(4096 * 8);
     int* aidx = (int*)alloc((size_t)MAXA * 4);
-    int* alab = (int*)alloc((size_t)MAXA * 4);
-    float* afe = (float*)alloc((size_t)MAXA * DD * 4);
     u32* featsH = (u32*)alloc((size_t)N * DD * 2);
     u8* ci8 = (u8*)alloc((size_t)N);
     if (ws_size < off) continue;
@@ -984,34 +919,26 @@
 
     k_top5A<<<dim3(NBLKA), dim3(256), 0, stream>>>(gt, labeled, RK, outA, ci8, N);
     k_top5B<<<dim3(LBN), dim3(256), 0, stream>>>(outA, rescue, top5F, NBLKA);
-    k_top5A_resc<<<dim3(NBLKA), dim3(256), 0, stream>>>(gt, labeled, RK, rescue, outA, N);
-    k_top5B_resc<<<dim3(LBN), dim3(256), 0, stream>>>(outA, rescue, top5F, NBLKA);
+    k_top5resc<<<dim3(1), dim3(1024), 0, stream>>>(gt, labeled, RK, rescue, top5F, N);
 
     uint2* featsH2 = (uint2*)featsH;
     k_normT<<<dim3(4096), dim3(256), 0, stream>>>((const float4*)feats, featsH2, N, Z3);
     k_initcentT<<<dim3(1), dim3(LBN * KMX * DD), 0, stream>>>(featsH, top5F, cent, N);
     for (int it = 0; it < KIT; ++it) {
       k_assignW2<<<dim3(NBAS), dim3(256), 0, stream>>>(featsH2, ci8, cent, part, N, NBAS);
-      k_redupdT<<<dim3(660), dim3(256), 0, stream>>>(part, cent, sums, kcnt, rescue + 2, NBAS);
-      k_fixempty<<<dim3(1), dim3(1024), 0, stream>>>(featsH, gt, labeled, RK, rescue + 2, cent, it, N);
+      k_redupdT<<<dim3(660), dim3(256), 0, stream>>>(part, cent, sums, kcnt, rescue + 2,
+                                                      tickets + it, featsH, gt, labeled, RK,
+                                                      it, N, NBAS);
     }
     k_anchor_final<<<dim3(LBN), dim3(64), 0, stream>>>(cent, sums, kcnt, protn, labeled, anchor_acc);
 
-    k_anchsel<<<dim3(2048), dim3(256), 0, stream>>>(pseudo, RK, cand4k, st, N);
-    k_selmode<<<dim3(1), dim3(64), 0, stream>>>(st, rescue);
-    k_svinit<<<dim3(1024), dim3(256), 0, stream>>>(pseudo, RK, rescue, sv, hist3, N);
-    k_scan<<<dim3(1), dim3(256), 0, stream>>>(hist3, st, rescue, 0);
-    k_hist12<<<dim3(1024), dim3(256), 0, stream>>>(sv, hist3 + 2048, st, rescue, 1, N);
-    k_scan<<<dim3(1), dim3(256), 0, stream>>>(hist3 + 2048, st, rescue, 1);
-    k_hist12<<<dim3(1024), dim3(256), 0, stream>>>(sv, hist3 + 4096, st, rescue, 2, N);
-    k_scan<<<dim3(1), dim3(256), 0, stream>>>(hist3 + 4096, st, rescue, 2);
-    k_gather<<<dim3(1024), dim3(256), 0, stream>>>(sv, st, rescue, cand, N);
-    k_sortsel<<<dim3(1), dim3(1024), 0, stream>>>(cand, st, rescue, aidx);
+    k_anchsel<<<dim3(2048), dim3(256), 0, stream>>>(pseudo, RK, cand4k, st, rescue,
+                                                     tickets + KIT, N);
+    k_rescue<<<dim3(1), dim3(1024), 0, stream>>>(pseudo, RK, st, rescue, aidx, N);
     k_rank<<<dim3(ACAP / 256), dim3(256), 0, stream>>>(cand4k, st, rescue, aidx);
 
-    k_prepT<<<dim3(MAXA / 32), dim3(256), 0, stream>>>(featsH2, pseudo, st, aidx,
-                                                        (float4*)afe, alab, N);
-    k_triplet<<<dim3(MAXA / 256), dim3(256), 0, stream>>>(protn, afe, alab, st, RK, proto_acc);
+    k_triplet<<<dim3(MAXA / 256), dim3(256), 0, stream>>>(protn, featsH2, pseudo, aidx,
+                                                           st, RK, proto_acc, N);
 
     k_final<<<dim3(1), dim3(64), 0, stream>>>(anchor_acc, proto_acc, compact, out);
     return;
```

After: 739.3 us. 32.8% more time.
